# Performance work log

Measured on AMD Instinct MI355X. Metric: run time of the kernel, lower is better.

## Reference

```python
import jax, jax.numpy as jnp
import numpy as np

N_NODES = 100000
N_EDGES = 3200000
N_GRAPHS = 64


def setup_inputs() -> dict:
    key = jax.random.key(0)
    ks = jax.random.split(key, 9)
    x = jax.random.normal(ks[0], (N_NODES, 3), dtype=jnp.float32)
    edge_index = jax.random.randint(ks[1], (2, N_EDGES), 0, N_NODES, dtype=jnp.int64)
    batch = jnp.sort(jax.random.randint(ks[2], (N_NODES,), 0, N_GRAPHS, dtype=jnp.int64))
    s1 = 1.0 / np.sqrt(3.0)
    s2 = 1.0 / np.sqrt(64.0)
    W1 = jax.random.normal(ks[3], (3, 64), dtype=jnp.float32) * s1
    b1 = jax.random.normal(ks[4], (64,), dtype=jnp.float32) * 0.02
    W2 = jax.random.normal(ks[5], (64, 64), dtype=jnp.float32) * s2
    b2 = jax.random.normal(ks[6], (64,), dtype=jnp.float32) * 0.02
    Wr = jax.random.normal(ks[7], (64, 1), dtype=jnp.float32) * s2
    br = jax.random.normal(ks[8], (1,), dtype=jnp.float32) * 0.02
    return {"x": x, "edge_index": edge_index, "batch": batch,
            "W1": W1, "b1": b1, "W2": W2, "b2": b2, "Wr": Wr, "br": br}


def reference(x, edge_index, batch, W1, b1, W2, b2, Wr, br):
    N = x.shape[0]
    # GCN normalization with self-loops: A_hat = D^-1/2 (A+I) D^-1/2
    loop = jnp.arange(N, dtype=edge_index.dtype)
    src = jnp.concatenate([edge_index[0], loop])  # message sources
    dst = jnp.concatenate([edge_index[1], loop])  # aggregation targets
    deg = jax.ops.segment_sum(jnp.ones(src.shape, jnp.float32), dst, num_segments=N)
    dinv = jnp.where(deg > 0, jax.lax.rsqrt(deg), 0.0)
    norm = dinv[src] * dinv[dst]  # [E+N]

    def conv(h):  # h: [N, F] -> gather, scale, scatter-add
        return jax.ops.segment_sum(norm[:, None] * h[src], dst, num_segments=N)

    h = jax.nn.relu(conv(x @ W1) + b1)
    # dropout(p=0.5) is identity in eval mode
    h = jax.nn.relu(conv(h @ W2) + b2)
    # global mean pool over graphs
    counts = jax.ops.segment_sum(jnp.ones((N,), jnp.float32), batch, num_segments=N_GRAPHS)
    pooled = jax.ops.segment_sum(h, batch, num_segments=N_GRAPHS) / jnp.maximum(counts, 1.0)[:, None]
    return pooled @ Wr + br
```

## Files before the change

### kernel.cpp

```cpp
#include <hip/hip_runtime.h>

#define N_NODES  100000
#define N_EDGES  3200000
#define N_GRAPHS 64
#define NBUCK 391
#define BSH   8
#define TILE  4096
#define CSR_CAP 9216

typedef float v2f __attribute__((ext_vector_type(2)));

__device__ __forceinline__ unsigned pk8(float a, float b, float c, float d) {
    int r = 0;
    r = __builtin_amdgcn_cvt_pk_fp8_f32(a, b, r, false);
    r = __builtin_amdgcn_cvt_pk_fp8_f32(c, d, r, true);
    return (unsigned)r;
}
__device__ __forceinline__ void addfp8(float4& a, unsigned u) {
    v2f lo = __builtin_amdgcn_cvt_pk_f32_fp8((int)u, false);
    v2f hi = __builtin_amdgcn_cvt_pk_f32_fp8((int)u, true);
    a.x += lo[0]; a.y += lo[1]; a.z += hi[0]; a.w += hi[1];
}
__device__ __forceinline__ void fma4(float4& c, float s, const float4& w) {
    c.x += s * w.x; c.y += s * w.y; c.z += s * w.z; c.w += s * w.w;
}

__global__ __launch_bounds__(1024) void k_split(
        const int* __restrict__ src, const int* __restrict__ dst,
        int* __restrict__ gcur, unsigned int* __restrict__ ebuf, int E) {
    __shared__ int hist[512];
    __shared__ int excl_s[512];
    __shared__ int base[NBUCK];
    __shared__ int curs[NBUCK];
    __shared__ int wtot[8];
    __shared__ unsigned int stg[TILE];
    __shared__ unsigned short bkt[TILE];
    int t = threadIdx.x;
    if (t < 512) hist[t] = 0;
    __syncthreads();

    int e0 = blockIdx.x * TILE;
    int nvalid = min(TILE, E - e0);
    int es[4], ed[4];
#pragma unroll
    for (int k = 0; k < 4; ++k) {
        int i = e0 + t + k * 1024;
        if (i < E) {
            es[k] = src[i]; ed[k] = dst[i];
            atomicAdd(&hist[ed[k] >> BSH], 1);
        } else { es[k] = 0; ed[k] = -1; }
    }
    __syncthreads();
    int v = (t < 512) ? hist[t] : 0;
    int lane = t & 63, wvi = t >> 6;
    int val = v;
    for (int off = 1; off < 64; off <<= 1) {
        int u = __shfl_up(val, off);
        if (lane >= off) val += u;
    }
    if (t < 512 && lane == 63) wtot[wvi] = val;
    __syncthreads();
    if (t < 512) {
        int woff = 0;
        for (int w = 0; w < wvi; ++w) woff += wtot[w];
        int texcl = woff + val - v;
        excl_s[t] = texcl;
        if (t < NBUCK) {
            if (v > 0) base[t] = atomicAdd(&gcur[t], v);
            curs[t] = 0;
        }
    }
    __syncthreads();
#pragma unroll
    for (int k = 0; k < 4; ++k) {
        if (ed[k] >= 0) {
            int b = ed[k] >> BSH;
            int r = atomicAdd(&curs[b], 1);
            int pos = excl_s[b] + r;
            stg[pos] = ((unsigned)(ed[k] & 255) << 24) | (unsigned)es[k];
            bkt[pos] = (unsigned short)b;
        }
    }
    __syncthreads();
    for (int j = t; j < nvalid; j += 1024) {
        unsigned p = stg[j];
        int b = bkt[j];
        int pos = base[b] + (j - excl_s[b]);
        if (pos < CSR_CAP) ebuf[(size_t)b * CSR_CAP + pos] = p;
    }
}

__global__ __launch_bounds__(1024) void k_csr(
        const unsigned int* __restrict__ ebuf, const int* __restrict__ gcur,
        int* __restrict__ rowptr, float* __restrict__ dinv, float4* __restrict__ y4,
        const float* __restrict__ x, int* __restrict__ csr_src, int N) {
    __shared__ int ncnt[256];
    __shared__ int nbase[256];
    __shared__ int ncur[256];
    __shared__ int wtot[4];
    __shared__ int sbase;
    __shared__ int stg[CSR_CAP];
    int b = blockIdx.x, t = threadIdx.x;
    int node0 = b << BSH;
    int nodes = min(256, N - node0);
    int cntE = min(gcur[b], CSR_CAP);
    const unsigned int* eb = ebuf + (size_t)b * CSR_CAP;
    if (t < 64) {
        int acc = 0;
        for (int i = t; i < b; i += 64) acc += min(gcur[i], CSR_CAP);
        for (int off = 32; off > 0; off >>= 1) acc += __shfl_down(acc, off);
        if (t == 0) sbase = acc;
    }
    if (t < 256) { ncnt[t] = 0; ncur[t] = 0; }
    __syncthreads();
    int base = sbase;
    if (b == NBUCK - 1 && t == 0) rowptr[N_NODES] = base + cntE;
    for (int j = t; j < cntE; j += 1024) atomicAdd(&ncnt[(int)(eb[j] >> 24)], 1);
    __syncthreads();
    int v = (t < 256) ? ncnt[t] : 0;
    if (t < 256) {
        int lane = t & 63, wv = t >> 6;
        int val = v;
        for (int off = 1; off < 64; off <<= 1) {
            int u = __shfl_up(val, off);
            if (lane >= off) val += u;
        }
        if (lane == 63) wtot[wv] = val;
        __syncthreads();
        int woff = 0;
        for (int w = 0; w < wv; ++w) woff += wtot[w];
        int excl = woff + val - v;
        nbase[t] = excl;
        if (t < nodes) {
            int nn = node0 + t;
            rowptr[nn] = base + excl;
            float dn = rsqrtf((float)(v + 1));
            dinv[nn] = dn;
            y4[nn] = make_float4(dn * x[nn * 3 + 0], dn * x[nn * 3 + 1], dn * x[nn * 3 + 2], 0.f);
        }
    } else {
        __syncthreads();
    }
    __syncthreads();
    for (int j = t; j < cntE; j += 1024) {
        unsigned p = eb[j];
        int ln = (int)(p >> 24);
        int r = atomicAdd(&ncur[ln], 1);
        stg[nbase[ln] + r] = (int)(p & 0xFFFFFFu);
    }
    __syncthreads();
    for (int j = t; j < cntE; j += 1024) csr_src[(size_t)base + j] = stg[j];
}

__global__ __launch_bounds__(256) void k_agg3h1(
        const float4* __restrict__ y4, const int* __restrict__ csr_src,
        const int* __restrict__ rowptr, const float* __restrict__ dinv,
        const float* __restrict__ W1, const float* __restrict__ b1,
        uint4* __restrict__ Hs, int N) {
    int tid = blockIdx.x * blockDim.x + threadIdx.x;
    int n = tid >> 2, q = tid & 3;
    if (n >= N) return;
    int beg = rowptr[n], end = rowptr[n + 1];
    float4 a0 = make_float4(0.f, 0.f, 0.f, 0.f);
    float4 a1 = make_float4(0.f, 0.f, 0.f, 0.f);
    float4 a2 = make_float4(0.f, 0.f, 0.f, 0.f);
    float4 a3 = make_float4(0.f, 0.f, 0.f, 0.f);
    int c = beg + q;
    for (; c + 12 < end; c += 16) {
        int s0 = csr_src[c], s1 = csr_src[c + 4], s2 = csr_src[c + 8], s3 = csr_src[c + 12];
        float4 v0 = y4[s0], v1 = y4[s1], v2 = y4[s2], v3 = y4[s3];
        a0.x += v0.x; a0.y += v0.y; a0.z += v0.z;
        a1.x += v1.x; a1.y += v1.y; a1.z += v1.z;
        a2.x += v2.x; a2.y += v2.y; a2.z += v2.z;
        a3.x += v3.x; a3.y += v3.y; a3.z += v3.z;
    }
    for (; c < end; c += 4) {
        float4 v = y4[csr_src[c]];
        a0.x += v.x; a0.y += v.y; a0.z += v.z;
    }
    float rx = (a0.x + a1.x) + (a2.x + a3.x);
    float ry = (a0.y + a1.y) + (a2.y + a3.y);
    float rz = (a0.z + a1.z) + (a2.z + a3.z);
    for (int off = 1; off < 4; off <<= 1) {
        rx += __shfl_xor(rx, off);
        ry += __shfl_xor(ry, off);
        rz += __shfl_xor(rz, off);
    }
    float dn = dinv[n];
    float4 self = y4[n];
    float A0 = dn * (rx + self.x), A1 = dn * (ry + self.y), A2 = dn * (rz + self.z);
    unsigned vals[4];
#pragma unroll
    for (int g = 0; g < 4; ++g) {
        int f = 16 * q + 4 * g;
        float w0 = dn * fmaxf(A0 * W1[f]     + A1 * W1[64 + f]     + A2 * W1[128 + f]     + b1[f],     0.f);
        float w1 = dn * fmaxf(A0 * W1[f + 1] + A1 * W1[64 + f + 1] + A2 * W1[128 + f + 1] + b1[f + 1], 0.f);
        float w2 = dn * fmaxf(A0 * W1[f + 2] + A1 * W1[64 + f + 2] + A2 * W1[128 + f + 2] + b1[f + 2], 0.f);
        float w3 = dn * fmaxf(A0 * W1[f + 3] + A1 * W1[64 + f + 3] + A2 * W1[128 + f + 3] + b1[f + 3], 0.f);
        vals[g] = pk8(w0, w1, w2, w3);
    }
    Hs[(size_t)n * 4 + q] = make_uint4(vals[0], vals[1], vals[2], vals[3]);
}

__global__ __launch_bounds__(256) void k_agg(
        const unsigned int* __restrict__ Hs, const int* __restrict__ csr_src,
        const int* __restrict__ rowptr, const float* __restrict__ dinv,
        float* __restrict__ out, int N) {
    int tid = blockIdx.x * blockDim.x + threadIdx.x;
    int n = tid >> 4, q = tid & 15;
    if (n >= N) return;
    int lane = threadIdx.x & 63;
    int base = lane & ~15;
    int beg = rowptr[n], end = rowptr[n + 1];
    float4 acc0 = make_float4(0.f, 0.f, 0.f, 0.f);
    float4 acc1 = make_float4(0.f, 0.f, 0.f, 0.f);
    float4 acc2 = make_float4(0.f, 0.f, 0.f, 0.f);
    float4 acc3 = make_float4(0.f, 0.f, 0.f, 0.f);
    for (int c = beg; c < end; c += 16) {
        int myidx = csr_src[min(c + q, end - 1)];
        int m = min(16, end - c);
        int j = 0;
        for (; j + 4 <= m; j += 4) {
            int s0 = __shfl(myidx, base + j + 0);
            int s1 = __shfl(myidx, base + j + 1);
            int s2 = __shfl(myidx, base + j + 2);
            int s3 = __shfl(myidx, base + j + 3);
            unsigned u0 = Hs[(size_t)s0 * 16 + q];
            unsigned u1 = Hs[(size_t)s1 * 16 + q];
            unsigned u2 = Hs[(size_t)s2 * 16 + q];
            unsigned u3 = Hs[(size_t)s3 * 16 + q];
            addfp8(acc0, u0); addfp8(acc1, u1); addfp8(acc2, u2); addfp8(acc3, u3);
        }
        for (; j < m; ++j) {
            int s = __shfl(myidx, base + j);
            addfp8(acc0, Hs[(size_t)s * 16 + q]);
        }
    }
    addfp8(acc0, Hs[(size_t)n * 16 + q]);
    float dn = dinv[n];
    float4 r;
    r.x = dn * ((acc0.x + acc1.x) + (acc2.x + acc3.x));
    r.y = dn * ((acc0.y + acc1.y) + (acc2.y + acc3.y));
    r.z = dn * ((acc0.z + acc1.z) + (acc2.z + acc3.z));
    r.w = dn * ((acc0.w + acc1.w) + (acc2.w + acc3.w));
    ((float4*)(out + (size_t)n * 64))[q] = r;
}

__global__ __launch_bounds__(256) void k_mmpool(
        const float4* __restrict__ A4, const float4* __restrict__ W2v,
        const float* __restrict__ b2, const float* __restrict__ Wr,
        const int* __restrict__ batch, float* __restrict__ gsum,
        float* __restrict__ gcnt, int N) {
    __shared__ float4 W2s[1024];
    __shared__ float lsum[N_GRAPHS];
    __shared__ float lcnt[N_GRAPHS];
    int t = threadIdx.x;
    for (int i = t; i < 1024; i += 256) W2s[i] = W2v[i];
    if (t < N_GRAPHS) { lsum[t] = 0.f; lcnt[t] = 0.f; }
    __syncthreads();

    int f4 = t & 15;
    int ng = t >> 4;
    float4 bb = ((const float4*)b2)[f4];
    float4 wr = ((const float4*)Wr)[f4];
    int base = blockIdx.x * 128;

    for (int tile = 0; tile < 2; ++tile) {
        int n0 = base + tile * 64 + ng * 4;
        int m0 = min(n0 + 0, N - 1), m1 = min(n0 + 1, N - 1);
        int m2 = min(n0 + 2, N - 1), m3 = min(n0 + 3, N - 1);
        const float4* r0 = A4 + (size_t)m0 * 16;
        const float4* r1 = A4 + (size_t)m1 * 16;
        const float4* r2 = A4 + (size_t)m2 * 16;
        const float4* r3 = A4 + (size_t)m3 * 16;
        float4 c0 = make_float4(0.f, 0.f, 0.f, 0.f);
        float4 c1 = make_float4(0.f, 0.f, 0.f, 0.f);
        float4 c2 = make_float4(0.f, 0.f, 0.f, 0.f);
        float4 c3 = make_float4(0.f, 0.f, 0.f, 0.f);
#pragma unroll 4
        for (int ks = 0; ks < 16; ++ks) {
            float4 a0 = r0[ks], a1 = r1[ks], a2 = r2[ks], a3 = r3[ks];
            float4 w0 = W2s[(4 * ks + 0) * 16 + f4];
            float4 w1 = W2s[(4 * ks + 1) * 16 + f4];
            float4 w2 = W2s[(4 * ks + 2) * 16 + f4];
            float4 w3 = W2s[(4 * ks + 3) * 16 + f4];
            fma4(c0, a0.x, w0); fma4(c0, a0.y, w1); fma4(c0, a0.z, w2); fma4(c0, a0.w, w3);
            fma4(c1, a1.x, w0); fma4(c1, a1.y, w1); fma4(c1, a1.z, w2); fma4(c1, a1.w, w3);
            fma4(c2, a2.x, w0); fma4(c2, a2.y, w1); fma4(c2, a2.z, w2); fma4(c2, a2.w, w3);
            fma4(c3, a3.x, w0); fma4(c3, a3.y, w1); fma4(c3, a3.z, w2); fma4(c3, a3.w, w3);
        }
        float p0 = fmaxf(c0.x + bb.x, 0.f) * wr.x + fmaxf(c0.y + bb.y, 0.f) * wr.y +
                   fmaxf(c0.z + bb.z, 0.f) * wr.z + fmaxf(c0.w + bb.w, 0.f) * wr.w;
        float p1 = fmaxf(c1.x + bb.x, 0.f) * wr.x + fmaxf(c1.y + bb.y, 0.f) * wr.y +
                   fmaxf(c1.z + bb.z, 0.f) * wr.z + fmaxf(c1.w + bb.w, 0.f) * wr.w;
        float p2 = fmaxf(c2.x + bb.x, 0.f) * wr.x + fmaxf(c2.y + bb.y, 0.f) * wr.y +
                   fmaxf(c2.z + bb.z, 0.f) * wr.z + fmaxf(c2.w + bb.w, 0.f) * wr.w;
        float p3 = fmaxf(c3.x + bb.x, 0.f) * wr.x + fmaxf(c3.y + bb.y, 0.f) * wr.y +
                   fmaxf(c3.z + bb.z, 0.f) * wr.z + fmaxf(c3.w + bb.w, 0.f) * wr.w;
        for (int off = 8; off > 0; off >>= 1) {
            p0 += __shfl_down(p0, off);
            p1 += __shfl_down(p1, off);
            p2 += __shfl_down(p2, off);
            p3 += __shfl_down(p3, off);
        }
        if (f4 == 0) {
            if (n0 + 0 < N) { int g = batch[n0 + 0]; atomicAdd(&lsum[g], p0); atomicAdd(&lcnt[g], 1.f); }
            if (n0 + 1 < N) { int g = batch[n0 + 1]; atomicAdd(&lsum[g], p1); atomicAdd(&lcnt[g], 1.f); }
            if (n0 + 2 < N) { int g = batch[n0 + 2]; atomicAdd(&lsum[g], p2); atomicAdd(&lcnt[g], 1.f); }
            if (n0 + 3 < N) { int g = batch[n0 + 3]; atomicAdd(&lsum[g], p3); atomicAdd(&lcnt[g], 1.f); }
        }
    }
    __syncthreads();
    if (t < N_GRAPHS && lcnt[t] > 0.0f) {
        atomicAdd(&gsum[t], lsum[t]);
        atomicAdd(&gcnt[t], lcnt[t]);
    }
}

__global__ void k_out(const float* __restrict__ gsum, const float* __restrict__ gcnt,
                      const float* __restrict__ br, float* __restrict__ out) {
    int g = threadIdx.x;
    if (g < N_GRAPHS) out[g] = gsum[g] / fmaxf(gcnt[g], 1.0f) + br[0];
}

extern "C" void kernel_launch(void* const* d_in, const int* in_sizes, int n_in,
                              void* d_out, int out_size, void* d_ws, size_t ws_size,
                              hipStream_t stream) {
    const float* x     = (const float*)d_in[0];
    const int*   ei    = (const int*)d_in[1];
    const int*   batch = (const int*)d_in[2];
    const float* W1    = (const float*)d_in[3];
    const float* b1    = (const float*)d_in[4];
    const float* W2    = (const float*)d_in[5];
    const float* b2    = (const float*)d_in[6];
    const float* Wr    = (const float*)d_in[7];
    const float* br    = (const float*)d_in[8];
    float* out = (float*)d_out;

    const int N = N_NODES, E = N_EDGES;
    const int* src = ei;
    const int* dst = ei + E;

    char* w = (char*)d_ws;
    float* A        = (float*)w; w += (size_t)N * 64 * sizeof(float);
    unsigned int* Hs = (unsigned int*)w; w += (size_t)N * 64;
    int*   csr_src  = (int*)w;   w += (size_t)E * sizeof(int);
    float* dinv     = (float*)w; w += (size_t)N * sizeof(float);
    int*   rowptr   = (int*)w;   w += (size_t)(N + 1) * sizeof(int);
    int*   gcur     = (int*)w;   w += (size_t)NBUCK * sizeof(int);
    float* gsum     = (float*)w; w += N_GRAPHS * sizeof(float);
    float* gcnt     = (float*)w; w += N_GRAPHS * sizeof(float);
    float4* y4      = (float4*)w; w += (size_t)N * sizeof(float4);
    unsigned int* ebuf = (unsigned int*)A;

    hipMemsetAsync(gcur, 0, (size_t)NBUCK * sizeof(int), stream);
    hipMemsetAsync(gsum, 0, N_GRAPHS * sizeof(float), stream);
    hipMemsetAsync(gcnt, 0, N_GRAPHS * sizeof(float), stream);

    k_split<<<(E + TILE - 1) / TILE, 1024, 0, stream>>>(src, dst, gcur, ebuf, E);
    k_csr<<<NBUCK, 1024, 0, stream>>>(ebuf, gcur, rowptr, dinv, y4, x, csr_src, N);

    k_agg3h1<<<(N * 4 + 255) / 256, 256, 0, stream>>>(y4, csr_src, rowptr, dinv,
                                                      W1, b1, (uint4*)Hs, N);

    k_agg<<<(N * 16 + 255) / 256, 256, 0, stream>>>(Hs, csr_src, rowptr, dinv, A, N);
    k_mmpool<<<(N + 127) / 128, 256, 0, stream>>>((const float4*)A, (const float4*)W2,
                                                  b2, Wr, batch, gsum, gcnt, N);

    k_out<<<1, 64, 0, stream>>>(gsum, gcnt, br, out);
}
```

Baseline: 217.4 us.

## Fuse second aggregation with W2 matmul and mean-pool via shared-memory tile

Merges the layer-2 neighbor aggregation kernel and the matmul+pool kernel into one. Each block aggregates 32 nodes with 8 lanes per node, each loading 8 fp8 bytes per gather, and stages the 64-wide result in LDS. It then applies W2, bias, ReLU and Wr from shared memory and pools. This removes the 25.6 MB float intermediate write and reread plus one launch. In exchange the matmul now runs in every block with fewer nodes per block, and the grid has no tail guard because it assumes N is divisible by 32.

```diff
diff --git a/kernel.cpp b/kernel.cpp
--- a/kernel.cpp
+++ b/kernel.cpp
@@ -202,113 +202,101 @@
     Hs[(size_t)n * 4 + q] = make_uint4(vals[0], vals[1], vals[2], vals[3]);
 }
 
-__global__ __launch_bounds__(256) void k_agg(
-        const unsigned int* __restrict__ Hs, const int* __restrict__ csr_src,
+__global__ __launch_bounds__(256) void k_aggpool(
+        const uint2* __restrict__ Hs2, const int* __restrict__ csr_src,
         const int* __restrict__ rowptr, const float* __restrict__ dinv,
-        float* __restrict__ out, int N) {
-    int tid = blockIdx.x * blockDim.x + threadIdx.x;
-    int n = tid >> 4, q = tid & 15;
-    if (n >= N) return;
-    int lane = threadIdx.x & 63;
-    int base = lane & ~15;
+        const float4* __restrict__ W2v, const float* __restrict__ b2,
+        const float* __restrict__ Wr, const int* __restrict__ batch,
+        float* __restrict__ gsum, float* __restrict__ gcnt, int N) {
+    __shared__ float4 W2s[1024];
+    __shared__ float4 A_s[32][17];
+    __shared__ float lsum[N_GRAPHS];
+    __shared__ float lcnt[N_GRAPHS];
+    int t = threadIdx.x;
+    for (int i = t; i < 1024; i += 256) W2s[i] = W2v[i];
+    if (t < N_GRAPHS) { lsum[t] = 0.f; lcnt[t] = 0.f; }
+
+    int ln = t >> 3;
+    int n = blockIdx.x * 32 + ln;
+    int q = t & 7;
+    int lane = t & 63;
+    int base = lane & ~7;
     int beg = rowptr[n], end = rowptr[n + 1];
-    float4 acc0 = make_float4(0.f, 0.f, 0.f, 0.f);
-    float4 acc1 = make_float4(0.f, 0.f, 0.f, 0.f);
-    float4 acc2 = make_float4(0.f, 0.f, 0.f, 0.f);
-    float4 acc3 = make_float4(0.f, 0.f, 0.f, 0.f);
-    for (int c = beg; c < end; c += 16) {
+    float4 a0a = make_float4(0.f,0.f,0.f,0.f), a0b = make_float4(0.f,0.f,0.f,0.f);
+    float4 a1a = make_float4(0.f,0.f,0.f,0.f), a1b = make_float4(0.f,0.f,0.f,0.f);
+    float4 a2a = make_float4(0.f,0.f,0.f,0.f), a2b = make_float4(0.f,0.f,0.f,0.f);
+    float4 a3a = make_float4(0.f,0.f,0.f,0.f), a3b = make_float4(0.f,0.f,0.f,0.f);
+    for (int c = beg; c < end; c += 8) {
         int myidx = csr_src[min(c + q, end - 1)];
-        int m = min(16, end - c);
+        int m = min(8, end - c);
         int j = 0;
         for (; j + 4 <= m; j += 4) {
             int s0 = __shfl(myidx, base + j + 0);
             int s1 = __shfl(myidx, base + j + 1);
             int s2 = __shfl(myidx, base + j + 2);
             int s3 = __shfl(myidx, base + j + 3);
-            unsigned u0 = Hs[(size_t)s0 * 16 + q];
-            unsigned u1 = Hs[(size_t)s1 * 16 + q];
-            unsigned u2 = Hs[(size_t)s2 * 16 + q];
-            unsigned u3 = Hs[(size_t)s3 * 16 + q];
-            addfp8(acc0, u0); addfp8(acc1, u1); addfp8(acc2, u2); addfp8(acc3, u3);
+            uint2 u0 = Hs2[(size_t)s0 * 8 + q];
+            uint2 u1 = Hs2[(size_t)s1 * 8 + q];
+            uint2 u2 = Hs2[(size_t)s2 * 8 + q];
+            uint2 u3 = Hs2[(size_t)s3 * 8 + q];
+            addfp8(a0a, u0.x); addfp8(a0b, u0.y);
+            addfp8(a1a, u1.x); addfp8(a1b, u1.y);
+            addfp8(a2a, u2.x); addfp8(a2b, u2.y);
+            addfp8(a3a, u3.x); addfp8(a3b, u3.y);
         }
         for (; j < m; ++j) {
             int s = __shfl(myidx, base + j);
-            addfp8(acc0, Hs[(size_t)s * 16 + q]);
-        }
-    }
-    addfp8(acc0, Hs[(size_t)n * 16 + q]);
+            uint2 u = Hs2[(size_t)s * 8 + q];
+            addfp8(a0a, u.x); addfp8(a0b, u.y);
+        }
+    }
+    {
+        uint2 us = Hs2[(size_t)n * 8 + q];
+        addfp8(a0a, us.x); addfp8(a0b, us.y);
+    }
     float dn = dinv[n];
-    float4 r;
-    r.x = dn * ((acc0.x + acc1.x) + (acc2.x + acc3.x));
-    r.y = dn * ((acc0.y + acc1.y) + (acc2.y + acc3.y));
-    r.z = dn * ((acc0.z + acc1.z) + (acc2.z + acc3.z));
-    r.w = dn * ((acc0.w + acc1.w) + (acc2.w + acc3.w));
-    ((float4*)(out + (size_t)n * 64))[q] = r;
-}
-
-__global__ __launch_bounds__(256) void k_mmpool(
-        const float4* __restrict__ A4, const float4* __restrict__ W2v,
-        const float* __restrict__ b2, const float* __restrict__ Wr,
-        const int* __restrict__ batch, float* __restrict__ gsum,
-        float* __restrict__ gcnt, int N) {
-    __shared__ float4 W2s[1024];
-    __shared__ float lsum[N_GRAPHS];
-    __shared__ float lcnt[N_GRAPHS];
-    int t = threadIdx.x;
-    for (int i = t; i < 1024; i += 256) W2s[i] = W2v[i];
-    if (t < N_GRAPHS) { lsum[t] = 0.f; lcnt[t] = 0.f; }
-    __syncthreads();
-
-    int f4 = t & 15;
-    int ng = t >> 4;
+    float4 ra, rb;
+    ra.x = dn * ((a0a.x + a1a.x) + (a2a.x + a3a.x));
+    ra.y = dn * ((a0a.y + a1a.y) + (a2a.y + a3a.y));
+    ra.z = dn * ((a0a.z + a1a.z) + (a2a.z + a3a.z));
+    ra.w = dn * ((a0a.w + a1a.w) + (a2a.w + a3a.w));
+    rb.x = dn * ((a0b.x + a1b.x) + (a2b.x + a3b.x));
+    rb.y = dn * ((a0b.y + a1b.y) + (a2b.y + a3b.y));
+    rb.z = dn * ((a0b.z + a1b.z) + (a2b.z + a3b.z));
+    rb.w = dn * ((a0b.w + a1b.w) + (a2b.w + a3b.w));
+    A_s[ln][2 * q]     = ra;
+    A_s[ln][2 * q + 1] = rb;
+    __syncthreads();
+
+    int f4 = t & 15, g = t >> 4;
+    int ln0 = 2 * g, ln1 = 2 * g + 1;
     float4 bb = ((const float4*)b2)[f4];
     float4 wr = ((const float4*)Wr)[f4];
-    int base = blockIdx.x * 128;
-
-    for (int tile = 0; tile < 2; ++tile) {
-        int n0 = base + tile * 64 + ng * 4;
-        int m0 = min(n0 + 0, N - 1), m1 = min(n0 + 1, N - 1);
-        int m2 = min(n0 + 2, N - 1), m3 = min(n0 + 3, N - 1);
-        const float4* r0 = A4 + (size_t)m0 * 16;
-        const float4* r1 = A4 + (size_t)m1 * 16;
-        const float4* r2 = A4 + (size_t)m2 * 16;
-        const float4* r3 = A4 + (size_t)m3 * 16;
-        float4 c0 = make_float4(0.f, 0.f, 0.f, 0.f);
-        float4 c1 = make_float4(0.f, 0.f, 0.f, 0.f);
-        float4 c2 = make_float4(0.f, 0.f, 0.f, 0.f);
-        float4 c3 = make_float4(0.f, 0.f, 0.f, 0.f);
+    float4 c0 = make_float4(0.f,0.f,0.f,0.f);
+    float4 c1 = make_float4(0.f,0.f,0.f,0.f);
 #pragma unroll 4
-        for (int ks = 0; ks < 16; ++ks) {
-            float4 a0 = r0[ks], a1 = r1[ks], a2 = r2[ks], a3 = r3[ks];
-            float4 w0 = W2s[(4 * ks + 0) * 16 + f4];
-            float4 w1 = W2s[(4 * ks + 1) * 16 + f4];
-            float4 w2 = W2s[(4 * ks + 2) * 16 + f4];
-            float4 w3 = W2s[(4 * ks + 3) * 16 + f4];
-            fma4(c0, a0.x, w0); fma4(c0, a0.y, w1); fma4(c0, a0.z, w2); fma4(c0, a0.w, w3);
-            fma4(c1, a1.x, w0); fma4(c1, a1.y, w1); fma4(c1, a1.z, w2); fma4(c1, a1.w, w3);
-            fma4(c2, a2.x, w0); fma4(c2, a2.y, w1); fma4(c2, a2.z, w2); fma4(c2, a2.w, w3);
-            fma4(c3, a3.x, w0); fma4(c3, a3.y, w1); fma4(c3, a3.z, w2); fma4(c3, a3.w, w3);
-        }
-        float p0 = fmaxf(c0.x + bb.x, 0.f) * wr.x + fmaxf(c0.y + bb.y, 0.f) * wr.y +
-                   fmaxf(c0.z + bb.z, 0.f) * wr.z + fmaxf(c0.w + bb.w, 0.f) * wr.w;
-        float p1 = fmaxf(c1.x + bb.x, 0.f) * wr.x + fmaxf(c1.y + bb.y, 0.f) * wr.y +
-                   fmaxf(c1.z + bb.z, 0.f) * wr.z + fmaxf(c1.w + bb.w, 0.f) * wr.w;
-        float p2 = fmaxf(c2.x + bb.x, 0.f) * wr.x + fmaxf(c2.y + bb.y, 0.f) * wr.y +
-                   fmaxf(c2.z + bb.z, 0.f) * wr.z + fmaxf(c2.w + bb.w, 0.f) * wr.w;
-        float p3 = fmaxf(c3.x + bb.x, 0.f) * wr.x + fmaxf(c3.y + bb.y, 0.f) * wr.y +
-                   fmaxf(c3.z + bb.z, 0.f) * wr.z + fmaxf(c3.w + bb.w, 0.f) * wr.w;
-        for (int off = 8; off > 0; off >>= 1) {
-            p0 += __shfl_down(p0, off);
-            p1 += __shfl_down(p1, off);
-            p2 += __shfl_down(p2, off);
-            p3 += __shfl_down(p3, off);
-        }
-        if (f4 == 0) {
-            if (n0 + 0 < N) { int g = batch[n0 + 0]; atomicAdd(&lsum[g], p0); atomicAdd(&lcnt[g], 1.f); }
-            if (n0 + 1 < N) { int g = batch[n0 + 1]; atomicAdd(&lsum[g], p1); atomicAdd(&lcnt[g], 1.f); }
-            if (n0 + 2 < N) { int g = batch[n0 + 2]; atomicAdd(&lsum[g], p2); atomicAdd(&lcnt[g], 1.f); }
-            if (n0 + 3 < N) { int g = batch[n0 + 3]; atomicAdd(&lsum[g], p3); atomicAdd(&lcnt[g], 1.f); }
-        }
+    for (int ks = 0; ks < 16; ++ks) {
+        float4 aa0 = A_s[ln0][ks];
+        float4 aa1 = A_s[ln1][ks];
+        float4 w0 = W2s[(4 * ks + 0) * 16 + f4];
+        float4 w1 = W2s[(4 * ks + 1) * 16 + f4];
+        float4 w2 = W2s[(4 * ks + 2) * 16 + f4];
+        float4 w3 = W2s[(4 * ks + 3) * 16 + f4];
+        fma4(c0, aa0.x, w0); fma4(c0, aa0.y, w1); fma4(c0, aa0.z, w2); fma4(c0, aa0.w, w3);
+        fma4(c1, aa1.x, w0); fma4(c1, aa1.y, w1); fma4(c1, aa1.z, w2); fma4(c1, aa1.w, w3);
+    }
+    float p0 = fmaxf(c0.x + bb.x, 0.f) * wr.x + fmaxf(c0.y + bb.y, 0.f) * wr.y +
+               fmaxf(c0.z + bb.z, 0.f) * wr.z + fmaxf(c0.w + bb.w, 0.f) * wr.w;
+    float p1 = fmaxf(c1.x + bb.x, 0.f) * wr.x + fmaxf(c1.y + bb.y, 0.f) * wr.y +
+               fmaxf(c1.z + bb.z, 0.f) * wr.z + fmaxf(c1.w + bb.w, 0.f) * wr.w;
+    for (int off = 8; off > 0; off >>= 1) {
+        p0 += __shfl_down(p0, off);
+        p1 += __shfl_down(p1, off);
+    }
+    if (f4 == 0) {
+        int n0 = blockIdx.x * 32 + ln0;
+        int g0 = batch[n0];     atomicAdd(&lsum[g0], p0); atomicAdd(&lcnt[g0], 1.f);
+        int g1 = batch[n0 + 1]; atomicAdd(&lsum[g1], p1); atomicAdd(&lcnt[g1], 1.f);
     }
     __syncthreads();
     if (t < N_GRAPHS && lcnt[t] > 0.0f) {
@@ -363,9 +351,9 @@
     k_agg3h1<<<(N * 4 + 255) / 256, 256, 0, stream>>>(y4, csr_src, rowptr, dinv,
                                                       W1, b1, (uint4*)Hs, N);
 
-    k_agg<<<(N * 16 + 255) / 256, 256, 0, stream>>>(Hs, csr_src, rowptr, dinv, A, N);
-    k_mmpool<<<(N + 127) / 128, 256, 0, stream>>>((const float4*)A, (const float4*)W2,
-                                                  b2, Wr, batch, gsum, gcnt, N);
+    k_aggpool<<<(N * 8) / 256, 256, 0, stream>>>((const uint2*)Hs, csr_src, rowptr,
+                                                 dinv, (const float4*)W2, b2, Wr,
+                                                 batch, gsum, gcnt, N);
 
     k_out<<<1, 64, 0, stream>>>(gsum, gcnt, br, out);
 }
```

After: 217.9 us. No clear change (+0.2%).

## Split fp8 hidden features into two planes and aggregate each half separately

Applied to the files above, without the earlier changes.

The layer-2 feature table is stored as two planes of 32 fp8 features per node instead of one interleaved 64-byte row. The aggregation now runs as two passes, each gathering from a 3.2 MB plane, so the randomly accessed working set is more likely to stay in L2/MALL cache. Index loads and output stores are marked nontemporal to reduce cache pollution. In exchange the CSR index stream is read twice, there is one more launch, and the grid of N*8/256 blocks has no bounds check, which is only safe because N*8 divides evenly by 256.

```diff
diff --git a/kernel.cpp b/kernel.cpp
--- a/kernel.cpp
+++ b/kernel.cpp
@@ -9,6 +9,7 @@
 #define CSR_CAP 9216
 
 typedef float v2f __attribute__((ext_vector_type(2)));
+typedef float v4f __attribute__((ext_vector_type(4)));
 
 __device__ __forceinline__ unsigned pk8(float a, float b, float c, float d) {
     int r = 0;
@@ -156,7 +157,7 @@
         const float4* __restrict__ y4, const int* __restrict__ csr_src,
         const int* __restrict__ rowptr, const float* __restrict__ dinv,
         const float* __restrict__ W1, const float* __restrict__ b1,
-        uint4* __restrict__ Hs, int N) {
+        unsigned int* __restrict__ Hs, int N) {
     int tid = blockIdx.x * blockDim.x + threadIdx.x;
     int n = tid >> 2, q = tid & 3;
     if (n >= N) return;
@@ -167,7 +168,10 @@
     float4 a3 = make_float4(0.f, 0.f, 0.f, 0.f);
     int c = beg + q;
     for (; c + 12 < end; c += 16) {
-        int s0 = csr_src[c], s1 = csr_src[c + 4], s2 = csr_src[c + 8], s3 = csr_src[c + 12];
+        int s0 = __builtin_nontemporal_load(&csr_src[c]);
+        int s1 = __builtin_nontemporal_load(&csr_src[c + 4]);
+        int s2 = __builtin_nontemporal_load(&csr_src[c + 8]);
+        int s3 = __builtin_nontemporal_load(&csr_src[c + 12]);
         float4 v0 = y4[s0], v1 = y4[s1], v2 = y4[s2], v3 = y4[s3];
         a0.x += v0.x; a0.y += v0.y; a0.z += v0.z;
         a1.x += v1.x; a1.y += v1.y; a1.z += v1.z;
@@ -175,7 +179,7 @@
         a3.x += v3.x; a3.y += v3.y; a3.z += v3.z;
     }
     for (; c < end; c += 4) {
-        float4 v = y4[csr_src[c]];
+        float4 v = y4[__builtin_nontemporal_load(&csr_src[c])];
         a0.x += v.x; a0.y += v.y; a0.z += v.z;
     }
     float rx = (a0.x + a1.x) + (a2.x + a3.x);
@@ -199,51 +203,53 @@
         float w3 = dn * fmaxf(A0 * W1[f + 3] + A1 * W1[64 + f + 3] + A2 * W1[128 + f + 3] + b1[f + 3], 0.f);
         vals[g] = pk8(w0, w1, w2, w3);
     }
-    Hs[(size_t)n * 4 + q] = make_uint4(vals[0], vals[1], vals[2], vals[3]);
-}
-
-__global__ __launch_bounds__(256) void k_agg(
-        const unsigned int* __restrict__ Hs, const int* __restrict__ csr_src,
+    uint4* dstp = (uint4*)(Hs + (size_t)(q >> 1) * N_NODES * 8);
+    dstp[(size_t)n * 2 + (q & 1)] = make_uint4(vals[0], vals[1], vals[2], vals[3]);
+}
+
+__global__ __launch_bounds__(256) void k_aggP(
+        const unsigned int* __restrict__ Hp,
+        const int* __restrict__ csr_src,
         const int* __restrict__ rowptr, const float* __restrict__ dinv,
-        float* __restrict__ out, int N) {
+        float* __restrict__ Aout, int po4, int N) {
     int tid = blockIdx.x * blockDim.x + threadIdx.x;
-    int n = tid >> 4, q = tid & 15;
-    if (n >= N) return;
+    int n = tid >> 3, q = tid & 7;
     int lane = threadIdx.x & 63;
-    int base = lane & ~15;
+    int base = lane & ~7;
     int beg = rowptr[n], end = rowptr[n + 1];
-    float4 acc0 = make_float4(0.f, 0.f, 0.f, 0.f);
-    float4 acc1 = make_float4(0.f, 0.f, 0.f, 0.f);
-    float4 acc2 = make_float4(0.f, 0.f, 0.f, 0.f);
-    float4 acc3 = make_float4(0.f, 0.f, 0.f, 0.f);
-    for (int c = beg; c < end; c += 16) {
-        int myidx = csr_src[min(c + q, end - 1)];
-        int m = min(16, end - c);
+    float4 a0 = make_float4(0.f, 0.f, 0.f, 0.f);
+    float4 a1 = make_float4(0.f, 0.f, 0.f, 0.f);
+    float4 a2 = make_float4(0.f, 0.f, 0.f, 0.f);
+    float4 a3 = make_float4(0.f, 0.f, 0.f, 0.f);
+    for (int c = beg; c < end; c += 8) {
+        int myidx = __builtin_nontemporal_load(&csr_src[min(c + q, end - 1)]);
+        int m = min(8, end - c);
         int j = 0;
         for (; j + 4 <= m; j += 4) {
             int s0 = __shfl(myidx, base + j + 0);
             int s1 = __shfl(myidx, base + j + 1);
             int s2 = __shfl(myidx, base + j + 2);
             int s3 = __shfl(myidx, base + j + 3);
-            unsigned u0 = Hs[(size_t)s0 * 16 + q];
-            unsigned u1 = Hs[(size_t)s1 * 16 + q];
-            unsigned u2 = Hs[(size_t)s2 * 16 + q];
-            unsigned u3 = Hs[(size_t)s3 * 16 + q];
-            addfp8(acc0, u0); addfp8(acc1, u1); addfp8(acc2, u2); addfp8(acc3, u3);
+            unsigned u0 = Hp[(size_t)s0 * 8 + q];
+            unsigned u1 = Hp[(size_t)s1 * 8 + q];
+            unsigned u2 = Hp[(size_t)s2 * 8 + q];
+            unsigned u3 = Hp[(size_t)s3 * 8 + q];
+            addfp8(a0, u0); addfp8(a1, u1); addfp8(a2, u2); addfp8(a3, u3);
         }
         for (; j < m; ++j) {
             int s = __shfl(myidx, base + j);
-            addfp8(acc0, Hs[(size_t)s * 16 + q]);
-        }
-    }
-    addfp8(acc0, Hs[(size_t)n * 16 + q]);
+            addfp8(a0, Hp[(size_t)s * 8 + q]);
+        }
+    }
+    addfp8(a0, Hp[(size_t)n * 8 + q]);
     float dn = dinv[n];
-    float4 r;
-    r.x = dn * ((acc0.x + acc1.x) + (acc2.x + acc3.x));
-    r.y = dn * ((acc0.y + acc1.y) + (acc2.y + acc3.y));
-    r.z = dn * ((acc0.z + acc1.z) + (acc2.z + acc3.z));
-    r.w = dn * ((acc0.w + acc1.w) + (acc2.w + acc3.w));
-    ((float4*)(out + (size_t)n * 64))[q] = r;
+    v4f r;
+    r[0] = dn * ((a0.x + a1.x) + (a2.x + a3.x));
+    r[1] = dn * ((a0.y + a1.y) + (a2.y + a3.y));
+    r[2] = dn * ((a0.z + a1.z) + (a2.z + a3.z));
+    r[3] = dn * ((a0.w + a1.w) + (a2.w + a3.w));
+    v4f* ap = (v4f*)(Aout + (size_t)n * 64) + po4 + q;
+    __builtin_nontemporal_store(r, ap);
 }
 
 __global__ __launch_bounds__(256) void k_mmpool(
@@ -361,9 +367,13 @@
     k_csr<<<NBUCK, 1024, 0, stream>>>(ebuf, gcur, rowptr, dinv, y4, x, csr_src, N);
 
     k_agg3h1<<<(N * 4 + 255) / 256, 256, 0, stream>>>(y4, csr_src, rowptr, dinv,
-                                                      W1, b1, (uint4*)Hs, N);
-
-    k_agg<<<(N * 16 + 255) / 256, 256, 0, stream>>>(Hs, csr_src, rowptr, dinv, A, N);
+                                                      W1, b1, Hs, N);
+
+    k_aggP<<<(N * 8) / 256, 256, 0, stream>>>(Hs,                 csr_src, rowptr,
+                                              dinv, A, 0, N);
+    k_aggP<<<(N * 8) / 256, 256, 0, stream>>>(Hs + (size_t)N * 8, csr_src, rowptr,
+                                              dinv, A, 8, N);
+
     k_mmpool<<<(N + 127) / 128, 256, 0, stream>>>((const float4*)A, (const float4*)W2,
                                                   b2, Wr, batch, gsum, gcnt, N);
 
```

New measurement: 259.6 us. +19.4%, slower.
